# Optimization experiments

Measured on AMD Instinct MI355X. Metric: run time of the kernel, lower is better.

The kernel has to match this reference:

```python
import jax, jax.numpy as jnp
import numpy as np

N_CLASSES = 80
TOPK = 13
ALPHA = 1.0
BETA = 6.0
EPS = 1e-9
BS, N_ANCHORS, N_MAX = 32, 8400, 100


def setup_inputs() -> dict:
    key = jax.random.key(0)
    k1, k2, k3, k4, k5, k6 = jax.random.split(key, 6)
    pred_scores = jax.random.uniform(k1, (BS, N_ANCHORS, N_CLASSES), dtype=jnp.float32)
    anchor_points = jax.random.uniform(k2, (N_ANCHORS, 2), dtype=jnp.float32) * 640.0
    # predicted boxes centered on anchor points (valid xyxy)
    wh = jax.random.uniform(k3, (BS, N_ANCHORS, 2), dtype=jnp.float32) * 100.0 + 4.0
    ctr = anchor_points[None]
    pred_bboxes = jnp.concatenate([ctr - wh / 2, ctr + wh / 2], axis=-1)
    gt_lt = jax.random.uniform(k4, (BS, N_MAX, 2), dtype=jnp.float32) * 500.0
    gt_wh = jax.random.uniform(k5, (BS, N_MAX, 2), dtype=jnp.float32) * 120.0 + 8.0
    gt_bboxes = jnp.concatenate([gt_lt, gt_lt + gt_wh], axis=-1)
    gt_labels = jax.random.randint(k6, (BS, N_MAX, 1), 0, N_CLASSES).astype(jnp.int32)
    mask_gt = jnp.ones((BS, N_MAX, 1), dtype=jnp.float32)
    return {"pred_scores": pred_scores, "pred_bboxes": pred_bboxes,
            "anchor_points": anchor_points, "gt_labels": gt_labels,
            "gt_bboxes": gt_bboxes, "mask_gt": mask_gt}


def _batch_iou(a, b):
    # a: [bs, n, 4], b: [bs, m, 4] (xyxy) -> [bs, n, m]
    lt = jnp.maximum(a[:, :, None, :2], b[:, None, :, :2])
    rb = jnp.minimum(a[:, :, None, 2:], b[:, None, :, 2:])
    wh = jnp.clip(rb - lt, 0.0)
    inter = wh[..., 0] * wh[..., 1]
    area_a = ((a[..., 2] - a[..., 0]) * (a[..., 3] - a[..., 1]))[:, :, None]
    area_b = ((b[..., 2] - b[..., 0]) * (b[..., 3] - b[..., 1]))[:, None, :]
    return inter / (area_a + area_b - inter + EPS)


def _assign(pred_scores, pred_bboxes, anchor_points, gt_labels, gt_bboxes, mask_gt):
    bs, n_anchors, n_classes = pred_scores.shape
    n_max = gt_bboxes.shape[1]
    labels = gt_labels[..., 0].astype(jnp.int32)  # [bs, n_max]

    # alignment metric: bbox_scores[b,g,a] = pred_scores[b,a,labels[b,g]]
    ps_t = jnp.swapaxes(pred_scores, 1, 2)  # [bs, C, n_anchors]
    bbox_scores = jnp.take_along_axis(ps_t, labels[:, :, None], axis=1)  # [bs, n_max, n_anchors]
    overlaps = _batch_iou(gt_bboxes, pred_bboxes)  # [bs, n_max, n_anchors]
    align_metric = jnp.power(bbox_scores, ALPHA) * jnp.power(overlaps, BETA)

    # anchor centers inside gt boxes
    ap = anchor_points[None, None, :, :]  # [1,1,n_anchors,2]
    deltas = jnp.concatenate(
        [ap - gt_bboxes[:, :, None, :2], gt_bboxes[:, :, None, 2:] - ap], axis=-1)
    is_in_gts = (deltas.min(axis=-1) > EPS).astype(align_metric.dtype)  # [bs,n_max,n_anchors]

    # topk candidate selection
    metrics = align_metric * is_in_gts
    _, topk_idxs = jax.lax.top_k(metrics, TOPK)  # [bs, n_max, TOPK]
    topk_mask = (mask_gt > 0)  # [bs, n_max, 1], broadcasts over TOPK
    topk_idxs = jnp.where(topk_mask, topk_idxs, 0)

    def count_row(idx):  # idx: [TOPK] -> anchor hit counts [n_anchors]
        return jnp.zeros((n_anchors,), jnp.int32).at[idx].add(1)
    counts = jax.vmap(jax.vmap(count_row))(topk_idxs)  # [bs, n_max, n_anchors]
    is_in_topk = jnp.where(counts > 1, 0, counts).astype(metrics.dtype)

    mask_pos = is_in_topk * is_in_gts * mask_gt  # [bs, n_max, n_anchors]

    # fix collisions: anchors assigned to multiple GTs keep the max-IoU GT
    mask_pos_sum = mask_pos.sum(axis=1)  # [bs, n_anchors]
    multi = mask_pos_sum[:, None, :] > 1
    is_max_overlaps = jax.nn.one_hot(overlaps.argmax(axis=1), n_max, axis=1,
                                     dtype=mask_pos.dtype)  # [bs, n_max, n_anchors]
    mask_pos = jnp.where(multi, is_max_overlaps, mask_pos)
    mask_pos_sum = mask_pos.sum(axis=1)
    assigned_gt_idx = mask_pos.argmax(axis=1)  # [bs, n_anchors]

    # final assignments via flattened gather
    flat_idx = assigned_gt_idx + jnp.arange(bs, dtype=jnp.int32)[:, None] * n_max
    assigned_labels = labels.reshape(-1)[flat_idx]  # [bs, n_anchors]
    assigned_bboxes = gt_bboxes.reshape(-1, 4)[flat_idx]  # [bs, n_anchors, 4]
    assigned_labels = jnp.where(assigned_labels < 0, 0, assigned_labels)
    assigned_scores = jax.nn.one_hot(assigned_labels, n_classes, dtype=pred_scores.dtype)
    pos = mask_pos_sum > 0
    assigned_scores = jnp.where(pos[..., None], assigned_scores, 0.0)
    assigned_labels = jnp.where(pos, assigned_labels, n_classes)

    # normalize scores by alignment metric
    align_metric = align_metric * mask_pos
    pos_align = align_metric.max(axis=-1, keepdims=True)  # [bs, n_max, 1]
    pos_overlaps = (overlaps * mask_pos).max(axis=-1, keepdims=True)
    norm = (align_metric * pos_overlaps / (pos_align + EPS)).max(axis=1)[..., None]  # [bs,n_anchors,1]
    assigned_scores = assigned_scores * norm

    return assigned_labels, assigned_bboxes, assigned_scores, pos


def reference(pred_scores, pred_bboxes, anchor_points, gt_labels, gt_bboxes, mask_gt):
    return _assign(pred_scores, pred_bboxes, anchor_points, gt_labels, gt_bboxes, mask_gt)
```

## Files before the change

### kernel.cpp

```cpp
#include <hip/hip_runtime.h>

#define BS 32
#define NA 8400
#define NMAX 100
#define NC 80
#define TOPK 13
#define EPSF 1e-9f
#define CAP 1024

#define OFF_LBL  0
#define OFF_BOX  (BS*NA)
#define OFF_SCR  (BS*NA + BS*NA*4)
#define OFF_POS  (BS*NA + BS*NA*4 + BS*NA*NC)

__device__ __forceinline__ float iou_fn(float gx1, float gy1, float gx2, float gy2,
                                        float px1, float py1, float px2, float py2) {
    float lx = fmaxf(gx1, px1), ly = fmaxf(gy1, py1);
    float rx = fminf(gx2, px2), ry = fminf(gy2, py2);
    float w = fmaxf(rx - lx, 0.f), h = fmaxf(ry - ly, 0.f);
    float inter = w * h;
    float aa = (gx2 - gx1) * (gy2 - gy1);
    float ab = (px2 - px1) * (py2 - py1);
    return inter / (aa + ab - inter + EPSF);
}

__global__ __launch_bounds__(256) void topk_kernel(
    const float* __restrict__ pred_scores,
    const float* __restrict__ pred_bboxes,
    const float* __restrict__ anchor_points,
    const int*   __restrict__ gt_labels,
    const float* __restrict__ gt_bboxes,
    const float* __restrict__ mask_gt,
    unsigned int* __restrict__ claims)
{
    int row = blockIdx.x;
    int b = row / NMAX, j = row % NMAX;
    if (mask_gt[row] <= 0.f) return;

    __shared__ unsigned long long cand[CAP];
    __shared__ unsigned short aidx[CAP];
    __shared__ int ncand;

    int t = threadIdx.x;
    if (t == 0) ncand = 0;
    __syncthreads();

    const float* gb = gt_bboxes + (size_t)row * 4;
    float gx1 = gb[0], gy1 = gb[1], gx2 = gb[2], gy2 = gb[3];
    int lab = gt_labels[row];

    const float2* ap2 = (const float2*)anchor_points;
    for (int a = t; a < NA; a += 256) {
        float2 ap = ap2[a];
        bool ing = (ap.x - gx1 > EPSF) && (ap.y - gy1 > EPSF) &&
                   (gx2 - ap.x > EPSF) && (gy2 - ap.y > EPSF);
        if (ing) {
            int pos = atomicAdd(&ncand, 1);
            if (pos < CAP) aidx[pos] = (unsigned short)a;
        }
    }
    __syncthreads();
    int n = ncand < CAP ? ncand : CAP;

    const float4* pb4 = (const float4*)pred_bboxes;
    for (int p = t; p < n; p += 256) {
        int a = aidx[p];
        float4 pb = pb4[b * NA + a];
        float iou = iou_fn(gx1, gy1, gx2, gy2, pb.x, pb.y, pb.z, pb.w);
        float s = pred_scores[((size_t)b * NA + a) * NC + lab];
        float i2 = iou * iou;
        float m = s * (i2 * i2 * i2);
        cand[p] = (m > 0.f)
                    ? (((unsigned long long)__float_as_uint(m) << 32) |
                       (unsigned int)(NA - a))
                    : 0ULL;
    }
    __syncthreads();

    if (t >= 64) return;

    unsigned long long loc[TOPK];
    #pragma unroll
    for (int i = 0; i < TOPK; i++) loc[i] = 0ULL;
    for (int p = t; p < n; p += 64) {
        unsigned long long k = cand[p];
        #pragma unroll
        for (int i = 0; i < TOPK; i++) {
            if (k > loc[i]) { unsigned long long tmp = loc[i]; loc[i] = k; k = tmp; }
        }
    }

    int head = 0;
    for (int r = 0; r < TOPK; r++) {
        unsigned long long h = (head < TOPK) ? loc[head] : 0ULL;
        unsigned long long m = h;
        #pragma unroll
        for (int s = 32; s > 0; s >>= 1) {
            unsigned long long o = __shfl_xor(m, s, 64);
            m = o > m ? o : m;
        }
        if (m == 0ULL) break;
        unsigned long long ball = __ballot(h == m);
        int winner = (int)__builtin_ctzll(ball);
        if (t == winner) {
            head++;
            int a = NA - (int)(unsigned int)(m & 0xFFFFFFFFULL);
            atomicAdd(&claims[b * NA + a], (1u << 16) | (unsigned int)j);
        }
    }
}

__global__ __launch_bounds__(256) void resolve_kernel(
    const float* __restrict__ pred_scores,
    const float* __restrict__ pred_bboxes,
    const int*   __restrict__ gt_labels,
    const float* __restrict__ gt_bboxes,
    const unsigned int* __restrict__ claims,
    int* __restrict__ assigned_j, float* __restrict__ a_align,
    unsigned int* __restrict__ pa_bits, unsigned int* __restrict__ po_bits)
{
    __shared__ float4 gtb[NMAX];
    __shared__ int    glab[NMAX];
    int b = blockIdx.y;
    int t = threadIdx.x;
    if (t < NMAX) {
        gtb[t]  = ((const float4*)gt_bboxes)[b * NMAX + t];
        glab[t] = gt_labels[b * NMAX + t];
    }
    __syncthreads();

    int ai = blockIdx.x * 256 + t;
    if (ai >= NA) return;
    int idx = b * NA + ai;
    unsigned int pk = claims[idx];
    if (pk == 0u) { assigned_j[idx] = -1; a_align[idx] = 0.f; return; }

    float4 pb = ((const float4*)pred_bboxes)[idx];

    int js;
    if ((pk >> 16) == 1u) {
        js = (int)(pk & 0xFFFFu);
    } else {
        float best = -1.f; js = 0;
        for (int j = 0; j < NMAX; j++) {
            float4 g = gtb[j];
            float v = iou_fn(g.x, g.y, g.z, g.w, pb.x, pb.y, pb.z, pb.w);
            if (v > best) { best = v; js = j; }
        }
    }
    float4 g = gtb[js];
    float iou = iou_fn(g.x, g.y, g.z, g.w, pb.x, pb.y, pb.z, pb.w);
    int lab = glab[js];
    float s = pred_scores[(size_t)idx * NC + lab];
    float i2 = iou * iou;
    float align = s * (i2 * i2 * i2);
    assigned_j[idx] = js; a_align[idx] = align;
    atomicMax(&pa_bits[b * NMAX + js], __float_as_uint(align));
    atomicMax(&po_bits[b * NMAX + js], __float_as_uint(iou));
}

__global__ __launch_bounds__(256) void finalize_kernel(
    const int*   __restrict__ gt_labels,
    const float* __restrict__ gt_bboxes,
    const int* __restrict__ assigned_j,
    const float* __restrict__ a_align,
    const unsigned int* __restrict__ pa_bits, const unsigned int* __restrict__ po_bits,
    float* __restrict__ out)
{
    int t = threadIdx.x;
    int idx = blockIdx.x * 256 + t;
    int b = idx / NA;
    int js = assigned_j[idx];
    bool pos = js >= 0;
    int j0 = pos ? js : 0;
    int lab = gt_labels[b * NMAX + j0];

    out[OFF_LBL + idx] = pos ? (float)lab : (float)NC;

    float4 gb = ((const float4*)gt_bboxes)[b * NMAX + j0];
    ((float4*)(out + OFF_BOX))[idx] = gb;

    out[OFF_POS + idx] = pos ? 1.f : 0.f;

    float4* sc = (float4*)(out + OFF_SCR + (size_t)blockIdx.x * 256 * NC);
    float4 z = make_float4(0.f, 0.f, 0.f, 0.f);
    #pragma unroll
    for (int i = 0; i < 256 * NC / 4 / 256; i++)
        sc[t + i * 256] = z;
    __syncthreads();

    if (pos) {
        float pa = __uint_as_float(pa_bits[b * NMAX + js]);
        float po = __uint_as_float(po_bits[b * NMAX + js]);
        float norm = a_align[idx] * po / (pa + EPSF);
        out[OFF_SCR + (size_t)idx * NC + lab] = norm;
    }
}

extern "C" void kernel_launch(void* const* d_in, const int* in_sizes, int n_in,
                              void* d_out, int out_size, void* d_ws, size_t ws_size,
                              hipStream_t stream) {
    const float* pred_scores   = (const float*)d_in[0];
    const float* pred_bboxes   = (const float*)d_in[1];
    const float* anchor_points = (const float*)d_in[2];
    const int*   gt_labels     = (const int*)d_in[3];
    const float* gt_bboxes     = (const float*)d_in[4];
    const float* mask_gt       = (const float*)d_in[5];

    char* ws = (char*)d_ws;
    const size_t NBA = (size_t)BS * NA;
    unsigned int* claims   = (unsigned int*)(ws);
    unsigned int* pa_bits  = (unsigned int*)(ws + NBA * 4);
    unsigned int* po_bits  = (unsigned int*)(ws + NBA * 4 + (size_t)BS * NMAX * 4);
    int*   assigned_j = (int*)(ws + NBA * 4 + (size_t)BS * NMAX * 8);
    float* a_align    = (float*)(ws + NBA * 8 + (size_t)BS * NMAX * 8);

    float* out = (float*)d_out;

    hipMemsetAsync(claims, 0, NBA * 4 + (size_t)BS * NMAX * 8, stream);

    topk_kernel<<<BS * NMAX, 256, 0, stream>>>(
        pred_scores, pred_bboxes, anchor_points, gt_labels, gt_bboxes, mask_gt, claims);

    dim3 rgrid((NA + 255) / 256, BS);
    resolve_kernel<<<rgrid, 256, 0, stream>>>(
        pred_scores, pred_bboxes, gt_labels, gt_bboxes, claims,
        assigned_j, a_align, pa_bits, po_bits);

    finalize_kernel<<<(int)(NBA / 256), 256, 0, stream>>>(
        gt_labels, gt_bboxes, assigned_j, a_align, pa_bits, po_bits, out);
}
```

Baseline: 242.8 us.

## Bin anchors into y-strips so each GT scans only overlapping strips

Adds a single-block kernel that buckets anchor points into 64 horizontal strips by y coordinate, storing the sorted points and their original indices. The top-k kernel then tests only anchors in the strips the GT box spans, instead of scanning all 8400 anchors for each of the 3200 GT rows. It also replaces the per-hit shared atomic with a wavefront ballot and one atomic per wave. The cost is an extra serial single-block launch, and candidate order in shared memory changes, though ties are still broken by anchor index.

```diff
diff --git a/kernel.cpp b/kernel.cpp
--- a/kernel.cpp
+++ b/kernel.cpp
@@ -7,6 +7,8 @@
 #define TOPK 13
 #define EPSF 1e-9f
 #define CAP 1024
+#define NSTRIP 64
+#define STRIP_INV 0.1f
 
 #define OFF_LBL  0
 #define OFF_BOX  (BS*NA)
@@ -24,13 +26,49 @@
     return inter / (aa + ab - inter + EPSF);
 }
 
+__global__ __launch_bounds__(256) void bin_kernel(
+    const float* __restrict__ anchor_points,
+    int* __restrict__ strip_off, float2* __restrict__ sAP, int* __restrict__ sIdx)
+{
+    __shared__ int cnt[NSTRIP];
+    __shared__ int cur[NSTRIP];
+    int t = threadIdx.x;
+    if (t < NSTRIP) cnt[t] = 0;
+    __syncthreads();
+    const float2* ap2 = (const float2*)anchor_points;
+    for (int a = t; a < NA; a += 256) {
+        int s = (int)(ap2[a].y * STRIP_INV);
+        s = s < 0 ? 0 : (s > NSTRIP - 1 ? NSTRIP - 1 : s);
+        atomicAdd(&cnt[s], 1);
+    }
+    __syncthreads();
+    if (t == 0) {
+        int acc = 0;
+        for (int s = 0; s < NSTRIP; s++) {
+            cur[s] = acc; strip_off[s] = acc; acc += cnt[s];
+        }
+        strip_off[NSTRIP] = acc;
+    }
+    __syncthreads();
+    for (int a = t; a < NA; a += 256) {
+        float2 p = ap2[a];
+        int s = (int)(p.y * STRIP_INV);
+        s = s < 0 ? 0 : (s > NSTRIP - 1 ? NSTRIP - 1 : s);
+        int pos = atomicAdd(&cur[s], 1);
+        sAP[pos] = p;
+        sIdx[pos] = a;
+    }
+}
+
 __global__ __launch_bounds__(256) void topk_kernel(
     const float* __restrict__ pred_scores,
     const float* __restrict__ pred_bboxes,
-    const float* __restrict__ anchor_points,
     const int*   __restrict__ gt_labels,
     const float* __restrict__ gt_bboxes,
     const float* __restrict__ mask_gt,
+    const int*   __restrict__ strip_off,
+    const float2* __restrict__ sAP,
+    const int*   __restrict__ sIdx,
     unsigned int* __restrict__ claims)
 {
     int row = blockIdx.x;
@@ -49,14 +87,30 @@
     float gx1 = gb[0], gy1 = gb[1], gx2 = gb[2], gy2 = gb[3];
     int lab = gt_labels[row];
 
-    const float2* ap2 = (const float2*)anchor_points;
-    for (int a = t; a < NA; a += 256) {
-        float2 ap = ap2[a];
-        bool ing = (ap.x - gx1 > EPSF) && (ap.y - gy1 > EPSF) &&
-                   (gx2 - ap.x > EPSF) && (gy2 - ap.y > EPSF);
-        if (ing) {
-            int pos = atomicAdd(&ncand, 1);
-            if (pos < CAP) aidx[pos] = (unsigned short)a;
+    int s_lo = (int)(gy1 * STRIP_INV); s_lo = s_lo < 0 ? 0 : (s_lo > NSTRIP-1 ? NSTRIP-1 : s_lo);
+    int s_hi = (int)(gy2 * STRIP_INV); s_hi = s_hi < 0 ? 0 : (s_hi > NSTRIP-1 ? NSTRIP-1 : s_hi);
+    int lo = strip_off[s_lo], hi = strip_off[s_hi + 1];
+
+    int lane = t & 63;
+    for (int base = lo; base < hi; base += 256) {
+        int p = base + t;
+        bool hit = false;
+        int a = 0;
+        if (p < hi) {
+            float2 ap = sAP[p];
+            a = sIdx[p];
+            hit = (ap.x - gx1 > EPSF) && (ap.y - gy1 > EPSF) &&
+                  (gx2 - ap.x > EPSF) && (gy2 - ap.y > EPSF);
+        }
+        unsigned long long m = __ballot(hit);
+        if (m != 0ULL) {
+            int basepos = 0;
+            if (lane == 0) basepos = atomicAdd(&ncand, __popcll(m));
+            basepos = __shfl(basepos, 0, 64);
+            if (hit) {
+                int my = basepos + __popcll(m & ((1ULL << lane) - 1ULL));
+                if (my < CAP) aidx[my] = (unsigned short)a;
+            }
         }
     }
     __syncthreads();
@@ -214,13 +268,20 @@
     unsigned int* po_bits  = (unsigned int*)(ws + NBA * 4 + (size_t)BS * NMAX * 4);
     int*   assigned_j = (int*)(ws + NBA * 4 + (size_t)BS * NMAX * 8);
     float* a_align    = (float*)(ws + NBA * 8 + (size_t)BS * NMAX * 8);
+    size_t off5 = NBA * 12 + (size_t)BS * NMAX * 8;
+    int*    strip_off = (int*)(ws + off5);
+    float2* sAP       = (float2*)(ws + off5 + 512);
+    int*    sIdx      = (int*)(ws + off5 + 512 + (size_t)NA * 8);
 
     float* out = (float*)d_out;
 
     hipMemsetAsync(claims, 0, NBA * 4 + (size_t)BS * NMAX * 8, stream);
 
+    bin_kernel<<<1, 256, 0, stream>>>(anchor_points, strip_off, sAP, sIdx);
+
     topk_kernel<<<BS * NMAX, 256, 0, stream>>>(
-        pred_scores, pred_bboxes, anchor_points, gt_labels, gt_bboxes, mask_gt, claims);
+        pred_scores, pred_bboxes, gt_labels, gt_bboxes, mask_gt,
+        strip_off, sAP, sIdx, claims);
 
     dim3 rgrid((NA + 255) / 256, BS);
     resolve_kernel<<<rgrid, 256, 0, stream>>>(
```

Result: no change. 243.8 us (+0.4%).
